# Kernel optimization log

Measured on AMD Instinct MI355X. Metric: run time of the kernel, lower is better.

## Reference

```python
import jax, jax.numpy as jnp
import numpy as np

D_MODEL = 1024
N_HEADS = 16
D_KV = 64
INNER = N_HEADS * D_KV  # 1024


def setup_inputs() -> dict:
    key = jax.random.key(0)
    ks = jax.random.split(key, 6)
    B, SV, ST = 4, 1024, 1024
    vis = jax.random.normal(ks[0], (B, SV, D_MODEL), dtype=jnp.float32)
    txt = jax.random.normal(ks[1], (B, ST, D_MODEL), dtype=jnp.float32)
    s = 0.02
    Wq = jax.random.normal(ks[2], (D_MODEL, INNER), dtype=jnp.float32) * s
    Wk = jax.random.normal(ks[3], (D_MODEL, INNER), dtype=jnp.float32) * s
    Wv = jax.random.normal(ks[4], (D_MODEL, INNER), dtype=jnp.float32) * s
    Wo = jax.random.normal(ks[5], (INNER, D_MODEL), dtype=jnp.float32) * s
    return {"vis_hidden_states": vis, "txt_hidden_states": txt,
            "Wq": Wq, "Wk": Wk, "Wv": Wv, "Wo": Wo}


def _split_heads(x):
    # [B, S, INNER] -> [B, H, S, Dk]
    B, S, _ = x.shape
    return x.reshape(B, S, N_HEADS, D_KV).transpose(0, 2, 1, 3)


def _merge_heads(x):
    # [B, H, S, Dk] -> [B, S, INNER]
    B, H, S, Dk = x.shape
    return x.transpose(0, 2, 1, 3).reshape(B, S, H * Dk)


def reference(vis_hidden_states, txt_hidden_states, Wq, Wk, Wv, Wo):
    # T5-style attention: NO 1/sqrt(d) scaling, no biases.
    q = _split_heads(vis_hidden_states @ Wq)   # [B,H,Sv,Dk]
    k = _split_heads(txt_hidden_states @ Wk)   # [B,H,St,Dk]
    v = _split_heads(txt_hidden_states @ Wv)   # [B,H,St,Dk]
    v2 = _split_heads(vis_hidden_states @ Wv)  # [B,H,Sv,Dk]

    scores = jnp.einsum('bhqd,bhkd->bhqk', q, k)  # [B,H,Sv,St]
    attn = jax.nn.softmax(scores.astype(jnp.float32), axis=-1).astype(scores.dtype)

    vis_out = jnp.einsum('bhqk,bhkd->bhqd', attn, v)   # softmax-normalized over k
    txt_out = jnp.einsum('bhqk,bhqd->bhkd', attn, v2)  # transposed attn, NOT renormalized

    vis_out = _merge_heads(vis_out) @ Wo  # [B,Sv,D]
    txt_out = _merge_heads(txt_out) @ Wo  # [B,St,D]
    return vis_out, txt_out
```

## Files before the change

kernel.cpp:

```cpp
#include <hip/hip_runtime.h>

typedef unsigned short u16;
typedef unsigned int u32;
typedef __bf16 bf16x8 __attribute__((ext_vector_type(8)));
typedef float f32x4 __attribute__((ext_vector_type(4)));
typedef u16 u16x4 __attribute__((ext_vector_type(4)));
typedef __attribute__((address_space(1))) void* as1_t;
typedef __attribute__((address_space(3))) void* as3_t;

#define LOG2E 1.4426950408889634f
#define MFMA(a,b,c) __builtin_amdgcn_mfma_f32_16x16x32_bf16(a,b,c,0,0,0)

__device__ __forceinline__ u16 f2bf(float f){
  u32 u = __float_as_uint(f);
  return (u16)((u + 0x7FFFu + ((u >> 16) & 1u)) >> 16);
}
__device__ __forceinline__ float bf2f(u16 x){
  return __uint_as_float(((u32)x) << 16);
}
#if __has_builtin(__builtin_amdgcn_cvt_pk_bf16_f32)
__device__ __forceinline__ u16x4 pk4(float a, float b, float c, float d){
  auto lo = __builtin_amdgcn_cvt_pk_bf16_f32(a,b);
  auto hi = __builtin_amdgcn_cvt_pk_bf16_f32(c,d);
  union { u16x4 v; u32 w[2]; } u;
  u.w[0] = __builtin_bit_cast(u32, lo);
  u.w[1] = __builtin_bit_cast(u32, hi);
  return u.v;
}
#else
__device__ __forceinline__ u16x4 pk4(float a, float b, float c, float d){
  u16x4 r = { f2bf(a), f2bf(b), f2bf(c), f2bf(d) };
  return r;
}
#endif
__device__ __forceinline__ void gld16(const u16* gp, u16* lp){
  __builtin_amdgcn_global_load_lds((as1_t)(u16*)gp, (as3_t)lp, 16, 0, 0);
}

#define SBAR  __builtin_amdgcn_s_barrier()
#define SCHB  __builtin_amdgcn_sched_barrier(0)
#define SP1   __builtin_amdgcn_s_setprio(1)
#define SP0   __builtin_amdgcn_s_setprio(0)
#define WAITL0 asm volatile("s_waitcnt lgkmcnt(0)" ::: "memory")
#define WV2 asm volatile("s_waitcnt vmcnt(2)" ::: "memory")
#define WV8 asm volatile("s_waitcnt vmcnt(8)" ::: "memory")

__global__ void prep_kernel(const float* __restrict__ vis, u16* __restrict__ vis16,
                            const float* __restrict__ txt, u16* __restrict__ txt16,
                            const float* __restrict__ Wq, const float* __restrict__ Wk,
                            const float* __restrict__ Wv, const float* __restrict__ Wo,
                            u16* __restrict__ T0, u16* __restrict__ T1,
                            u16* __restrict__ T2, u16* __restrict__ T3,
                            u16* __restrict__ T4){
  int bid = blockIdx.x;
  if(bid < 8192){
    const float* src = (bid < 4096) ? vis : txt;
    u16* dst = (bid < 4096) ? vis16 : txt16;
    int idx = ((bid & 4095)*256 + threadIdx.x)*4;
    float4 v = *(const float4*)(src + idx);
    *(u16x4*)(dst + idx) = pk4(v.x, v.y, v.z, v.w);
    return;
  }
  int rr = bid - 8192;
  int wi = rr >> 8, tile = rr & 255;
  const float* W; u16* WT;
  switch(wi){
    case 0: W = Wq; WT = T0; break;
    case 1: W = Wv; WT = T1; break;
    case 2: W = Wk; WT = T2; break;
    case 3: W = Wv; WT = T3; break;
    default: W = Wo; WT = T4; break;
  }
  __shared__ u16 t[64][65];
  int bn = (tile & 15)*64, bk = (tile >> 4)*64;
  int c = threadIdx.x & 63, r0 = threadIdx.x >> 6;
  #pragma unroll
  for(int j=0;j<64;j+=4){
    int r = r0 + j;
    t[r][c] = f2bf(W[(bk + r)*1024 + bn + c]);
  }
  __syncthreads();
  #pragma unroll
  for(int j=0;j<64;j+=4){
    int r = r0 + j;
    WT[(bn + r)*1024 + bk + c] = t[c][r];
  }
}

#define STG(G, gbase, dsto, kk) { \
    _Pragma("unroll") \
    for(int ii=0;ii<4;ii++){ \
      int slot_ = ii*512 + tid; int r_ = slot_ >> 3, cs_ = slot_ & 7; \
      gld16((G) + (size_t)((gbase) + r_)*1024 + (kk) + ((cs_ ^ (r_ & 7)) << 3), \
            lds + (dsto) + (ii*512 + (w << 6))*8); } }

#define LDA_(bo, mh) { \
    _Pragma("unroll") \
    for(int q_=0;q_<4;q_++){ \
      int ro_ = (bo) + arow + (((mh)*4 + q_) << 10); \
      af[q_][0] = *(const bf16x8*)(lds + ro_ + sx0); \
      af[q_][1] = *(const bf16x8*)(lds + ro_ + sx1); } }

#define LDB_(bo, nh, bfv) { \
    _Pragma("unroll") \
    for(int j_=0;j_<2;j_++){ \
      int ro_ = (bo) + brow + (((nh)*2 + j_) << 10); \
      bfv[j_][0] = *(const bf16x8*)(lds + ro_ + sx0); \
      bfv[j_][1] = *(const bf16x8*)(lds + ro_ + sx1); } }

#define MM_N(mh, bfv, nh) { \
    _Pragma("unroll") \
    for(int q_=0;q_<4;q_++) \
      _Pragma("unroll") \
      for(int j_=0;j_<2;j_++){ \
        int ai_ = ((mh)*4+q_)*4 + (nh)*2+j_; \
        acc[ai_] = MFMA(af[q_][0], bfv[j_][0], acc[ai_]); \
        acc[ai_] = MFMA(af[q_][1], bfv[j_][1], acc[ai_]); } }

#define MM_T(mh, bfv, nh) { \
    _Pragma("unroll") \
    for(int q_=0;q_<4;q_++) \
      _Pragma("unroll") \
      for(int j_=0;j_<2;j_++){ \
        int ai_ = ((nh)*2+j_)*8 + (mh)*4+q_; \
        acc[ai_] = MFMA(bfv[j_][0], af[q_][0], acc[ai_]); \
        acc[ai_] = MFMA(bfv[j_][1], af[q_][1], acc[ai_]); } }

#define TILE_BODY(bufo, ts, MM) { \
    LDA_(bufo, 0); LDB_(bufo, 0, bfv0); \
    SBAR; WAITL0; SCHB; SP1; MM(0, bfv0, 0); SP0; SBAR; \
    LDB_(bufo, 1, bfv1); \
    SBAR; WAITL0; SCHB; SP1; MM(0, bfv1, 1); SP0; SBAR; \
    LDA_(bufo, 1); \
    SBAR; WAITL0; SCHB; SP1; MM(1, bfv1, 1); SP0; SBAR; \
    STG(A , bm, (bufo)        , ts); \
    STG(Bt, bn, (bufo) + 16384, ts); \
    SCHB; SP1; MM(1, bfv0, 0); SP0; \
    WV8; SBAR; }

__global__ __launch_bounds__(512, 2)
void proj_gemm_kernel(const u16* __restrict__ Avis, const u16* __restrict__ Atxt,
                      const u16* __restrict__ Wvis, const u16* __restrict__ Wtxt,
                      u16* __restrict__ Qb, u16* __restrict__ V2t,
                      u16* __restrict__ Kb, u16* __restrict__ Vt)
{
  const u16 *A, *Bt; u16 *Cn, *Ct;
  if(blockIdx.z == 0){ A = Avis; Bt = Wvis; Cn = Qb; Ct = V2t; }
  else               { A = Atxt; Bt = Wtxt; Cn = Kb; Ct = Vt;  }
  __shared__ u16 lds[65536];
  const int tid = threadIdx.x, w = tid >> 6, lane = tid & 63;
  const int quad = lane >> 4, cl = lane & 15;
  const int wr = w >> 2, wc = w & 3;
  const int bm = blockIdx.x*256, bn = blockIdx.y*256;
  const int sx0 = ((quad    ) ^ (cl & 7)) << 3;
  const int sx1 = ((quad + 4) ^ (cl & 7)) << 3;
  const int arow = ((wr << 7) + cl) << 6;
  const int brow = (((wc << 6) + cl) << 6) + 16384;

  f32x4 acc[32];
  #pragma unroll
  for(int a=0;a<32;a++){ f32x4 z = {0.f,0.f,0.f,0.f}; acc[a] = z; }
  bf16x8 af[4][2], bfv0[2][2], bfv1[2][2];

  STG(A , bm, 0,     0);  STG(Bt, bn, 16384, 0);
  STG(A , bm, 32768, 64); STG(Bt, bn, 32768+16384, 64);
  WV8; SBAR;

  if(bn < 1024){
    for(int tt=0; tt<8; tt++){
      const int t0 = 2*tt;
      TILE_BODY(0,     ((t0+2)&15) << 6, MM_N);
      TILE_BODY(32768, ((t0+3)&15) << 6, MM_N);
    }
    #pragma unroll
    for(int mf=0; mf<8; mf++){
      int m0 = bm + wr*128 + mf*16 + quad*4;
      #pragma unroll
      for(int nf=0; nf<4; nf++){
        int n = bn + wc*64 + nf*16 + cl;
        int h = n >> 6, d = n & 63;
        #pragma unroll
        for(int i2=0;i2<4;i2++){
          int m = m0 + i2; int b = m >> 10, s = m & 1023;
          Cn[(((size_t)(b*16 + h)*1024 + s) << 6) + d] = f2bf(acc[mf*4+nf][i2]);
        }
      }
    }
  } else {
    for(int tt=0; tt<8; tt++){
      const int t0 = 2*tt;
      TILE_BODY(0,     ((t0+2)&15) << 6, MM_T);
      TILE_BODY(32768, ((t0+3)&15) << 6, MM_T);
    }
    const int bT = bm >> 10;
    const int sbase = (bm & 1023) + wr*128;
    #pragma unroll
    for(int nf=0; nf<4; nf++){
      #pragma unroll
      for(int i2=0;i2<4;i2++){
        int nn = (bn - 1024) + wc*64 + nf*16 + quad*4 + i2;
        int h = nn >> 6, d = nn & 63;
        u16* rowp = Ct + ((size_t)(bT*16 + h)*64 + d)*1024;
        #pragma unroll
        for(int mf=0; mf<8; mf++)
          rowp[sbase + mf*16 + cl] = f2bf(acc[nf*8+mf][i2]);
      }
    }
  }
}

#undef STG
#undef LDA_
#undef LDB_
#undef MM_N
#undef MM_T
#undef TILE_BODY

#define STGO(G, gbase, dsto, kk) { \
    _Pragma("unroll") \
    for(int ii=0;ii<4;ii++){ \
      int slot_ = ii*256 + tid; int r_ = slot_ >> 3, cs_ = slot_ & 7; \
      gld16((G) + (size_t)((gbase) + r_)*1024 + (kk) + ((cs_ ^ (r_ & 7)) << 3), \
            lds + (dsto) + (ii*256 + (w << 6))*8); } }

__global__ __launch_bounds__(256, 2)
void out_gemm_kernel(const u16* __restrict__ A, const u16* __restrict__ Bt,
                     float* __restrict__ Cf)
{
  __shared__ u16 lds[32768];
  const int tid = threadIdx.x, w = tid >> 6, lane = tid & 63;
  const int quad = lane >> 4, cl = lane & 15;
  const int wr = w >> 1, wc = w & 1;
  const int bm = blockIdx.x*128, bn = blockIdx.y*128;
  const int sx0 = ((quad    ) ^ (cl & 7)) << 3;
  const int sx1 = ((quad + 4) ^ (cl & 7)) << 3;
  const int arow = ((wr << 6) + cl) << 6;
  const int brow = (((wc << 6) + cl) << 6) + 8192;

  f32x4 acc[4][4];
  #pragma unroll
  for(int a=0;a<4;a++)
    #pragma unroll
    for(int b=0;b<4;b++){ f32x4 z = {0.f,0.f,0.f,0.f}; acc[a][b] = z; }
  bf16x8 af[4][2], bfv[4][2];

  STGO(A , bm, 0,    0);
  STGO(Bt, bn, 8192, 0);
  __syncthreads();

  #pragma unroll 2
  for(int t=0; t<16; ++t){
    const int c  = (t & 1) << 14;
    const int nb = c ^ 16384;
    if(t < 15){
      STGO(A , bm, nb,        (t+1) << 6);
      STGO(Bt, bn, nb + 8192, (t+1) << 6);
    }
    #pragma unroll
    for(int m=0;m<4;m++){
      int ro = c + arow + (m << 10);
      af[m][0] = *(const bf16x8*)(lds + ro + sx0);
      af[m][1] = *(const bf16x8*)(lds + ro + sx1);
    }
    #pragma unroll
    for(int n=0;n<4;n++){
      int ro = c + brow + (n << 10);
      bfv[n][0] = *(const bf16x8*)(lds + ro + sx0);
      bfv[n][1] = *(const bf16x8*)(lds + ro + sx1);
    }
    SP1;
    #pragma unroll
    for(int m=0;m<4;m++)
      #pragma unroll
      for(int n=0;n<4;n++){
        acc[m][n] = MFMA(af[m][0], bfv[n][0], acc[m][n]);
        acc[m][n] = MFMA(af[m][1], bfv[n][1], acc[m][n]);
      }
    SP0;
    __syncthreads();
  }

  #pragma unroll
  for(int mf=0; mf<4; mf++)
    #pragma unroll
    for(int nf=0; nf<4; nf++)
      #pragma unroll
      for(int i=0;i<4;i++){
        int m = bm + wr*64 + mf*16 + quad*4 + i;
        int n = bn + wc*64 + nf*16 + cl;
        Cf[(size_t)m*1024 + n] = acc[mf][nf][i];
      }
}
#undef STGO

__global__ __launch_bounds__(512, 4)
void attn_vis_kernel(const u16* __restrict__ Q, const u16* __restrict__ Kc,
                     const u16* __restrict__ Vt, u16* __restrict__ visA,
                     float* __restrict__ rl_g)
{
  __shared__ u16 lds[25600];
  u16* Pl  = lds;
  const int tid = threadIdx.x, w = tid>>6, lane = tid&63;
  const int quad = lane>>4, cl = lane&15;
  const int bh = blockIdx.x, q0 = blockIdx.y*128;
  const u16* Qh  = Q  + (size_t)bh*65536;
  const u16* Kh  = Kc + (size_t)bh*65536;
  const u16* Vth = Vt + (size_t)bh*65536;

  #pragma unroll
  for(int i=0;i<2;i++){
    int slot = i*512 + tid;
    int c = slot >> 7, r = slot & 127;
    gld16(Qh + (size_t)(q0 + r)*64 + c*8, Pl + slot*8);
  }
  __syncthreads();
  bf16x8 qf[2];
  #pragma unroll
  for(int kk=0;kk<2;kk++)
    qf[kk] = *(const bf16x8*)(Pl + ((kk*4+quad)*128 + w*16 + cl)*8);
  __syncthreads();

#define KVST(kt, buf) { \
    u16* B_ = lds + 9216 + (buf)*8192; \
    { int c_ = tid >> 6, r_ = tid & 63; \
      gld16(Kh + (size_t)((kt)*64 + r_)*64 + c_*8, B_ + tid*8); } \
    { int d_ = tid >> 3, ch_ = tid & 7; \
      gld16(Vth + (size_t)d_*1024 + (kt)*64 + ((ch_^(d_&7))*8), B_ + 4096 + tid*8); } }

  KVST(0, 0); KVST(1, 1);
  WV2; SBAR;

  float lrun = 0.f;
  f32x4 oacc[4];
  #pragma unroll
  for(int dt=0;dt<4;dt++){ f32x4 z = {0.f,0.f,0.f,0.f}; oacc[dt] = z; }

  for(int kt=0;kt<16;kt++){
    const int bb = kt & 1;
    u16* Kst = lds + 9216 + bb*8192;
    u16* Vst = Kst + 4096;
    #pragma unroll
    for(int mtk=0;mtk<4;mtk++){
      f32x4 s = {0.f,0.f,0.f,0.f};
      #pragma unroll
      for(int kk=0;kk<2;kk++){
        bf16x8 ka = *(const bf16x8*)(Kst + ((kk*4+quad)*64 + mtk*16 + cl)*8);
        s = MFMA(ka, qf[kk], s);
      }
      float p0 = __builtin_amdgcn_exp2f(s[0]*LOG2E);
      float p1 = __builtin_amdgcn_exp2f(s[1]*LOG2E);
      float p2 = __builtin_amdgcn_exp2f(s[2]*LOG2E);
      float p3 = __builtin_amdgcn_exp2f(s[3]*LOG2E);
      lrun += (p0+p1)+(p2+p3);
      *(u16x4*)(Pl + (w*16 + cl)*72 + mtk*16 + quad*4) = pk4(p0,p1,p2,p3);
    }
    bf16x8 pa[2];
    #pragma unroll
    for(int kk=0;kk<2;kk++)
      pa[kk] = *(const bf16x8*)(Pl + (w*16 + cl)*72 + kk*32 + quad*8);
    #pragma unroll
    for(int dt=0;dt<4;dt++){
      int d = dt*16 + cl;
      #pragma unroll
      for(int kk=0;kk<2;kk++){
        bf16x8 vb = *(const bf16x8*)(Vst + d*64 + (((kk*4+quad)^(d&7))*8));
        oacc[dt] = MFMA(pa[kk], vb, oacc[dt]);
      }
    }
    SBAR;
    const int nk = (kt < 14) ? kt + 2 : kt;
    KVST(nk, bb);
    WV2;
    SBAR;
  }
#undef KVST
  lrun += __shfl_xor(lrun, 16, 64);
  lrun += __shfl_xor(lrun, 32, 64);
  float rl = 1.f/lrun;
  if(quad == 0) rl_g[bh*1024 + q0 + w*16 + cl] = rl;
  const int b = bh >> 4, h = bh & 15;
  #pragma unroll
  for(int i=0;i<4;i++){
    float rr = __shfl(rl, quad*4 + i, 16);
    int q = q0 + w*16 + quad*4 + i;
    #pragma unroll
    for(int dt=0;dt<4;dt++)
      visA[(size_t)(b*1024 + q)*1024 + h*64 + dt*16 + cl] = f2bf(oacc[dt][i]*rr);
  }
}

__global__ __launch_bounds__(512, 4)
void attn_txt_kernel(const u16* __restrict__ Kc, const u16* __restrict__ Q,
                     const u16* __restrict__ V2t, const float* __restrict__ rl_g,
                     u16* __restrict__ txtA)
{
  __shared__ u16 lds[27648];
  u16* Pl  = lds;
  u16* rlL = lds + 25600;
  const float* rlF = (const float*)rlL;
  const int tid = threadIdx.x, w = tid>>6, lane = tid&63;
  const int quad = lane>>4, cl = lane&15;
  const int bh = blockIdx.x, k0 = blockIdx.y*128;
  const u16* Kh  = Kc  + (size_t)bh*65536;
  const u16* Qh  = Q   + (size_t)bh*65536;
  const u16* Vth = V2t + (size_t)bh*65536;

  #pragma unroll
  for(int i=0;i<2;i++){
    int slot = i*512 + tid;
    int c = slot >> 7, r = slot & 127;
    gld16(Kh + (size_t)(k0 + r)*64 + c*8, Pl + slot*8);
  }
  if(tid < 256)
    gld16((const u16*)(rl_g + (size_t)bh*1024) + tid*8, rlL + tid*8);
  __syncthreads();
  bf16x8 kb[2];
  #pragma unroll
  for(int kk=0;kk<2;kk++)
    kb[kk] = *(const bf16x8*)(Pl + ((kk*4+quad)*128 + w*16 + cl)*8);
  __syncthreads();

#define QVST(qt, buf) { \
    u16* B_ = lds + 9216 + (buf)*8192; \
    { int c_ = tid >> 6, r_ = tid & 63; \
      gld16(Qh + (size_t)((qt)*64 + r_)*64 + c_*8, B_ + tid*8); } \
    { int d_ = tid >> 3, ch_ = tid & 7; \
      gld16(Vth + (size_t)d_*1024 + (qt)*64 + ((ch_^(d_&7))*8), B_ + 4096 + tid*8); } }

  QVST(0, 0); QVST(1, 1);
  WV2; SBAR;

  f32x4 oacc[4];
  #pragma unroll
  for(int dt=0;dt<4;dt++){ f32x4 z = {0.f,0.f,0.f,0.f}; oacc[dt] = z; }

  for(int qt=0;qt<16;qt++){
    const int bb = qt & 1;
    u16* Qst = lds + 9216 + bb*8192;
    u16* Vst = Qst + 4096;
    f32x4 rv[4];
    #pragma unroll
    for(int mtq=0;mtq<4;mtq++)
      rv[mtq] = *(const f32x4*)(rlF + qt*64 + mtq*16 + quad*4);
    #pragma unroll
    for(int mtq=0;mtq<4;mtq++){
      f32x4 s = {0.f,0.f,0.f,0.f};
      #pragma unroll
      for(int kk=0;kk<2;kk++){
        bf16x8 qa = *(const bf16x8*)(Qst + ((kk*4+quad)*64 + mtq*16 + cl)*8);
        s = MFMA(qa, kb[kk], s);
      }
      float p0 = __builtin_amdgcn_exp2f(s[0]*LOG2E)*rv[mtq][0];
      float p1 = __builtin_amdgcn_exp2f(s[1]*LOG2E)*rv[mtq][1];
      float p2 = __builtin_amdgcn_exp2f(s[2]*LOG2E)*rv[mtq][2];
      float p3 = __builtin_amdgcn_exp2f(s[3]*LOG2E)*rv[mtq][3];
      *(u16x4*)(Pl + (w*16 + cl)*72 + mtq*16 + quad*4) = pk4(p0,p1,p2,p3);
    }
    bf16x8 pa[2];
    #pragma unroll
    for(int kk=0;kk<2;kk++)
      pa[kk] = *(const bf16x8*)(Pl + (w*16 + cl)*72 + kk*32 + quad*8);
    #pragma unroll
    for(int dt=0;dt<4;dt++){
      int d = dt*16 + cl;
      #pragma unroll
      for(int kk=0;kk<2;kk++){
        bf16x8 vb = *(const bf16x8*)(Vst + d*64 + (((kk*4+quad)^(d&7))*8));
        oacc[dt] = MFMA(pa[kk], vb, oacc[dt]);
      }
    }
    SBAR;
    const int nq = (qt < 14) ? qt + 2 : qt;
    QVST(nq, bb);
    WV2;
    SBAR;
  }
#undef QVST
  const int b = bh >> 4, h = bh & 15;
  #pragma unroll
  for(int i=0;i<4;i++){
    int k = k0 + w*16 + quad*4 + i;
    #pragma unroll
    for(int dt=0;dt<4;dt++)
      txtA[(size_t)(b*1024 + k)*1024 + h*64 + dt*16 + cl] = f2bf(oacc[dt][i]);
  }
}

extern "C" void kernel_launch(void* const* d_in, const int* in_sizes, int n_in,
                              void* d_out, int out_size, void* d_ws, size_t ws_size,
                              hipStream_t stream)
{
  const float* vis = (const float*)d_in[0];
  const float* txt = (const float*)d_in[1];
  const float* Wq  = (const float*)d_in[2];
  const float* Wk  = (const float*)d_in[3];
  const float* Wv  = (const float*)d_in[4];
  const float* Wo  = (const float*)d_in[5];
  float* out = (float*)d_out;

  char* ws = (char*)d_ws;
  const size_t MB = 1u << 20;
  u16* vis16 = (u16*)(ws + 0);
  u16* txt16 = (u16*)(ws + 8*MB);
  u16* Wvis  = (u16*)(ws + 16*MB);
  u16* Wtxt  = (u16*)(ws + 20*MB);
  u16* Qb    = (u16*)(ws + 24*MB);
  u16* Kb    = (u16*)(ws + 32*MB);
  u16* Vt    = (u16*)(ws + 40*MB);
  u16* V2t   = (u16*)(ws + 48*MB);
  float* rl_g = (float*)(ws + 56*MB);
  u16* WoT   = (u16*)(ws + 57*MB);
  u16* visA = vis16;  u16* txtA = txt16;

  prep_kernel<<<9472, 256, 0, stream>>>(vis, vis16, txt, txt16,
                                        Wq, Wk, Wv, Wo,
                                        Wvis, Wvis + 1048576, Wtxt, Wtxt + 1048576, WoT);
  proj_gemm_kernel<<<dim3(16,8,2), 512, 0, stream>>>(vis16, txt16, Wvis, Wtxt,
                                                     Qb, V2t, Kb, Vt);
  attn_vis_kernel<<<dim3(64,8), 512, 0, stream>>>(Qb, Kb, Vt, visA, rl_g);
  attn_txt_kernel<<<dim3(64,8), 512, 0, stream>>>(Kb, Qb, V2t, rl_g, txtA);
  out_gemm_kernel<<<dim3(64,8), 256, 0, stream>>>(visA, WoT, out);
}
```

Before: 209.5 us.

## Replace 256x256 projection GEMM with simpler 128x128 double-buffered tiling

The projection GEMM drops its 256x256-tile, 512-thread kernel with hand-placed sched/wait barriers. It now reuses the 128x128, 256-thread double-buffered loop from the output GEMM, launching four times as many blocks. The aim is better CU occupancy and load balance across the 1024-block grid. The cost is lower arithmetic reuse per block, more global traffic, and a full barrier every k-step without the fine-grained MFMA/LDS interleaving.

After: 221.4 us. 1.06x slower.

```diff
diff --git a/kernel.cpp b/kernel.cpp
--- a/kernel.cpp
+++ b/kernel.cpp
@@ -38,12 +38,9 @@
 }
 
 #define SBAR  __builtin_amdgcn_s_barrier()
-#define SCHB  __builtin_amdgcn_sched_barrier(0)
 #define SP1   __builtin_amdgcn_s_setprio(1)
 #define SP0   __builtin_amdgcn_s_setprio(0)
-#define WAITL0 asm volatile("s_waitcnt lgkmcnt(0)" ::: "memory")
 #define WV2 asm volatile("s_waitcnt vmcnt(2)" ::: "memory")
-#define WV8 asm volatile("s_waitcnt vmcnt(8)" ::: "memory")
 
 __global__ void prep_kernel(const float* __restrict__ vis, u16* __restrict__ vis16,
                             const float* __restrict__ txt, u16* __restrict__ txt16,
@@ -87,58 +84,14 @@
   }
 }
 
-#define STG(G, gbase, dsto, kk) { \
+#define STGO(G, gbase, dsto, kk) { \
     _Pragma("unroll") \
     for(int ii=0;ii<4;ii++){ \
-      int slot_ = ii*512 + tid; int r_ = slot_ >> 3, cs_ = slot_ & 7; \
+      int slot_ = ii*256 + tid; int r_ = slot_ >> 3, cs_ = slot_ & 7; \
       gld16((G) + (size_t)((gbase) + r_)*1024 + (kk) + ((cs_ ^ (r_ & 7)) << 3), \
-            lds + (dsto) + (ii*512 + (w << 6))*8); } }
-
-#define LDA_(bo, mh) { \
-    _Pragma("unroll") \
-    for(int q_=0;q_<4;q_++){ \
-      int ro_ = (bo) + arow + (((mh)*4 + q_) << 10); \
-      af[q_][0] = *(const bf16x8*)(lds + ro_ + sx0); \
-      af[q_][1] = *(const bf16x8*)(lds + ro_ + sx1); } }
-
-#define LDB_(bo, nh, bfv) { \
-    _Pragma("unroll") \
-    for(int j_=0;j_<2;j_++){ \
-      int ro_ = (bo) + brow + (((nh)*2 + j_) << 10); \
-      bfv[j_][0] = *(const bf16x8*)(lds + ro_ + sx0); \
-      bfv[j_][1] = *(const bf16x8*)(lds + ro_ + sx1); } }
-
-#define MM_N(mh, bfv, nh) { \
-    _Pragma("unroll") \
-    for(int q_=0;q_<4;q_++) \
-      _Pragma("unroll") \
-      for(int j_=0;j_<2;j_++){ \
-        int ai_ = ((mh)*4+q_)*4 + (nh)*2+j_; \
-        acc[ai_] = MFMA(af[q_][0], bfv[j_][0], acc[ai_]); \
-        acc[ai_] = MFMA(af[q_][1], bfv[j_][1], acc[ai_]); } }
-
-#define MM_T(mh, bfv, nh) { \
-    _Pragma("unroll") \
-    for(int q_=0;q_<4;q_++) \
-      _Pragma("unroll") \
-      for(int j_=0;j_<2;j_++){ \
-        int ai_ = ((nh)*2+j_)*8 + (mh)*4+q_; \
-        acc[ai_] = MFMA(bfv[j_][0], af[q_][0], acc[ai_]); \
-        acc[ai_] = MFMA(bfv[j_][1], af[q_][1], acc[ai_]); } }
-
-#define TILE_BODY(bufo, ts, MM) { \
-    LDA_(bufo, 0); LDB_(bufo, 0, bfv0); \
-    SBAR; WAITL0; SCHB; SP1; MM(0, bfv0, 0); SP0; SBAR; \
-    LDB_(bufo, 1, bfv1); \
-    SBAR; WAITL0; SCHB; SP1; MM(0, bfv1, 1); SP0; SBAR; \
-    LDA_(bufo, 1); \
-    SBAR; WAITL0; SCHB; SP1; MM(1, bfv1, 1); SP0; SBAR; \
-    STG(A , bm, (bufo)        , ts); \
-    STG(Bt, bn, (bufo) + 16384, ts); \
-    SCHB; SP1; MM(1, bfv0, 0); SP0; \
-    WV8; SBAR; }
-
-__global__ __launch_bounds__(512, 2)
+            lds + (dsto) + (ii*256 + (w << 6))*8); } }
+
+__global__ __launch_bounds__(256, 2)
 void proj_gemm_kernel(const u16* __restrict__ Avis, const u16* __restrict__ Atxt,
                       const u16* __restrict__ Wvis, const u16* __restrict__ Wtxt,
                       u16* __restrict__ Qb, u16* __restrict__ V2t,
@@ -147,34 +100,62 @@
   const u16 *A, *Bt; u16 *Cn, *Ct;
   if(blockIdx.z == 0){ A = Avis; Bt = Wvis; Cn = Qb; Ct = V2t; }
   else               { A = Atxt; Bt = Wtxt; Cn = Kb; Ct = Vt;  }
-  __shared__ u16 lds[65536];
+  __shared__ u16 lds[32768];
   const int tid = threadIdx.x, w = tid >> 6, lane = tid & 63;
   const int quad = lane >> 4, cl = lane & 15;
-  const int wr = w >> 2, wc = w & 3;
-  const int bm = blockIdx.x*256, bn = blockIdx.y*256;
+  const int wr = w >> 1, wc = w & 1;
+  const int bm = blockIdx.x*128, bn = blockIdx.y*128;
   const int sx0 = ((quad    ) ^ (cl & 7)) << 3;
   const int sx1 = ((quad + 4) ^ (cl & 7)) << 3;
-  const int arow = ((wr << 7) + cl) << 6;
-  const int brow = (((wc << 6) + cl) << 6) + 16384;
-
-  f32x4 acc[32];
-  #pragma unroll
-  for(int a=0;a<32;a++){ f32x4 z = {0.f,0.f,0.f,0.f}; acc[a] = z; }
-  bf16x8 af[4][2], bfv0[2][2], bfv1[2][2];
-
-  STG(A , bm, 0,     0);  STG(Bt, bn, 16384, 0);
-  STG(A , bm, 32768, 64); STG(Bt, bn, 32768+16384, 64);
-  WV8; SBAR;
+  const int arow = ((wr << 6) + cl) << 6;
+  const int brow = (((wc << 6) + cl) << 6) + 8192;
+
+  f32x4 acc[4][4];
+  #pragma unroll
+  for(int a=0;a<4;a++)
+    #pragma unroll
+    for(int b=0;b<4;b++){ f32x4 z = {0.f,0.f,0.f,0.f}; acc[a][b] = z; }
+  bf16x8 af[4][2], bfv[4][2];
+
+  STGO(A , bm, 0,    0);
+  STGO(Bt, bn, 8192, 0);
+  __syncthreads();
 
   if(bn < 1024){
-    for(int tt=0; tt<8; tt++){
-      const int t0 = 2*tt;
-      TILE_BODY(0,     ((t0+2)&15) << 6, MM_N);
-      TILE_BODY(32768, ((t0+3)&15) << 6, MM_N);
-    }
-    #pragma unroll
-    for(int mf=0; mf<8; mf++){
-      int m0 = bm + wr*128 + mf*16 + quad*4;
+    #pragma unroll 2
+    for(int t=0; t<16; ++t){
+      const int c  = (t & 1) << 14;
+      const int nb = c ^ 16384;
+      if(t < 15){
+        STGO(A , bm, nb,        (t+1) << 6);
+        STGO(Bt, bn, nb + 8192, (t+1) << 6);
+      }
+      #pragma unroll
+      for(int m=0;m<4;m++){
+        int ro = c + arow + (m << 10);
+        af[m][0] = *(const bf16x8*)(lds + ro + sx0);
+        af[m][1] = *(const bf16x8*)(lds + ro + sx1);
+      }
+      #pragma unroll
+      for(int n=0;n<4;n++){
+        int ro = c + brow + (n << 10);
+        bfv[n][0] = *(const bf16x8*)(lds + ro + sx0);
+        bfv[n][1] = *(const bf16x8*)(lds + ro + sx1);
+      }
+      SP1;
+      #pragma unroll
+      for(int m=0;m<4;m++)
+        #pragma unroll
+        for(int n=0;n<4;n++){
+          acc[m][n] = MFMA(af[m][0], bfv[n][0], acc[m][n]);
+          acc[m][n] = MFMA(af[m][1], bfv[n][1], acc[m][n]);
+        }
+      SP0;
+      __syncthreads();
+    }
+    #pragma unroll
+    for(int mf=0; mf<4; mf++){
+      int m0 = bm + wr*64 + mf*16 + quad*4;
       #pragma unroll
       for(int nf=0; nf<4; nf++){
         int n = bn + wc*64 + nf*16 + cl;
@@ -182,18 +163,44 @@
         #pragma unroll
         for(int i2=0;i2<4;i2++){
           int m = m0 + i2; int b = m >> 10, s = m & 1023;
-          Cn[(((size_t)(b*16 + h)*1024 + s) << 6) + d] = f2bf(acc[mf*4+nf][i2]);
+          Cn[(((size_t)(b*16 + h)*1024 + s) << 6) + d] = f2bf(acc[mf][nf][i2]);
         }
       }
     }
   } else {
-    for(int tt=0; tt<8; tt++){
-      const int t0 = 2*tt;
-      TILE_BODY(0,     ((t0+2)&15) << 6, MM_T);
-      TILE_BODY(32768, ((t0+3)&15) << 6, MM_T);
+    #pragma unroll 2
+    for(int t=0; t<16; ++t){
+      const int c  = (t & 1) << 14;
+      const int nb = c ^ 16384;
+      if(t < 15){
+        STGO(A , bm, nb,        (t+1) << 6);
+        STGO(Bt, bn, nb + 8192, (t+1) << 6);
+      }
+      #pragma unroll
+      for(int m=0;m<4;m++){
+        int ro = c + arow + (m << 10);
+        af[m][0] = *(const bf16x8*)(lds + ro + sx0);
+        af[m][1] = *(const bf16x8*)(lds + ro + sx1);
+      }
+      #pragma unroll
+      for(int n=0;n<4;n++){
+        int ro = c + brow + (n << 10);
+        bfv[n][0] = *(const bf16x8*)(lds + ro + sx0);
+        bfv[n][1] = *(const bf16x8*)(lds + ro + sx1);
+      }
+      SP1;
+      #pragma unroll
+      for(int n=0;n<4;n++)
+        #pragma unroll
+        for(int m=0;m<4;m++){
+          acc[n][m] = MFMA(bfv[n][0], af[m][0], acc[n][m]);
+          acc[n][m] = MFMA(bfv[n][1], af[m][1], acc[n][m]);
+        }
+      SP0;
+      __syncthreads();
     }
     const int bT = bm >> 10;
-    const int sbase = (bm & 1023) + wr*128;
+    const int sbase = (bm & 1023) + wr*64;
     #pragma unroll
     for(int nf=0; nf<4; nf++){
       #pragma unroll
@@ -202,26 +209,12 @@
         int h = nn >> 6, d = nn & 63;
         u16* rowp = Ct + ((size_t)(bT*16 + h)*64 + d)*1024;
         #pragma unroll
-        for(int mf=0; mf<8; mf++)
-          rowp[sbase + mf*16 + cl] = f2bf(acc[nf*8+mf][i2]);
-      }
-    }
-  }
-}
-
-#undef STG
-#undef LDA_
-#undef LDB_
-#undef MM_N
-#undef MM_T
-#undef TILE_BODY
-
-#define STGO(G, gbase, dsto, kk) { \
-    _Pragma("unroll") \
-    for(int ii=0;ii<4;ii++){ \
-      int slot_ = ii*256 + tid; int r_ = slot_ >> 3, cs_ = slot_ & 7; \
-      gld16((G) + (size_t)((gbase) + r_)*1024 + (kk) + ((cs_ ^ (r_ & 7)) << 3), \
-            lds + (dsto) + (ii*256 + (w << 6))*8); } }
+        for(int mf=0; mf<4; mf++)
+          rowp[sbase + mf*16 + cl] = f2bf(acc[nf][mf][i2]);
+      }
+    }
+  }
+}
 
 __global__ __launch_bounds__(256, 2)
 void out_gemm_kernel(const u16* __restrict__ A, const u16* __restrict__ Bt,
@@ -515,8 +508,8 @@
   prep_kernel<<<9472, 256, 0, stream>>>(vis, vis16, txt, txt16,
                                         Wq, Wk, Wv, Wo,
                                         Wvis, Wvis + 1048576, Wtxt, Wtxt + 1048576, WoT);
-  proj_gemm_kernel<<<dim3(16,8,2), 512, 0, stream>>>(vis16, txt16, Wvis, Wtxt,
-                                                     Qb, V2t, Kb, Vt);
+  proj_gemm_kernel<<<dim3(32,16,2), 256, 0, stream>>>(vis16, txt16, Wvis, Wtxt,
+                                                      Qb, V2t, Kb, Vt);
   attn_vis_kernel<<<dim3(64,8), 512, 0, stream>>>(Qb, Kb, Vt, visA, rl_g);
   attn_txt_kernel<<<dim3(64,8), 512, 0, stream>>>(Kb, Qb, V2t, rl_g, txtA);
   out_gemm_kernel<<<dim3(64,8), 256, 0, stream>>>(visA, WoT, out);
```
